# Performance work log

Hardware: AMD Instinct MI355X
Metric: run time of the kernel (lower is better)

The kernel has to match this reference:

```python
import jax, jax.numpy as jnp
import numpy as np
from jax import lax

SEQ_LEN = 1024
INPUT_DIM = 64
NUM_HIDDEN = 512
NUM_CLASSES = 10
BATCH = 256
SIGMA = 0.01


def setup_inputs() -> dict:
    key = jax.random.key(0)
    k_x, k_whx, k_whh, k_wph = jax.random.split(key, 4)
    x = jax.random.normal(k_x, (BATCH, SEQ_LEN, INPUT_DIM), dtype=jnp.float32)
    Whx = SIGMA * jax.random.normal(k_whx, (INPUT_DIM, NUM_HIDDEN), dtype=jnp.float32)
    Whh = SIGMA * jax.random.normal(k_whh, (NUM_HIDDEN, NUM_HIDDEN), dtype=jnp.float32)
    Wph = SIGMA * jax.random.normal(k_wph, (NUM_HIDDEN, NUM_CLASSES), dtype=jnp.float32)
    bh = jnp.zeros((NUM_HIDDEN, 1), dtype=jnp.float32)
    bp = jnp.zeros((NUM_CLASSES, 1), dtype=jnp.float32)
    return {"x": x, "Whx": Whx, "Whh": Whh, "Wph": Wph, "bh": bh, "bp": bp}


def reference(x, Whx, Whh, Wph, bh, bp):
    # x: [B, S, D]; h: [B, H]
    B = x.shape[0]
    H = Whh.shape[0]
    bh_row = bh[:, 0]  # per-hidden-unit bias (intended semantics of bh)
    bp_row = bp[:, 0]

    def step(h, xt):
        h_new = jnp.tanh(xt @ Whx + h @ Whh + bh_row)
        return h_new, None

    h0 = jnp.zeros((B, H), dtype=x.dtype)
    xs = jnp.swapaxes(x, 0, 1)  # [S, B, D] for scan over time
    h_final, _ = lax.scan(step, h0, xs)
    p = h_final @ Wph + bp_row  # [B, C]
    return p
```

## Files before the change

### kernel.cpp

```cpp
#include <hip/hip_runtime.h>
#include <hip/hip_bf16.h>
#include <hip/hip_fp8.h>
#include <cstdint>
#include <cstddef>


#define T_SEQ   1024
#define D_IN    64
#define H_DIM   512
#define NB      16
#define NBLK    16
#define NTW     4
#define KS_F16  10
#define KS_REG8 2
#define KS_LDS8 4
#define HSPLIT  320
#define APITCH  848
#define FP8OFF  640
#define ABUF_BYTES (2 * NB * APITCH)
#define WWAVE_BYTES (KS_LDS8 * 2 * 1024)
#define WLDS_BYTES (8 * WWAVE_BYTES)
#define SMEM_TOTAL (ABUF_BYTES + WLDS_BYTES)
#define WSCALE  256.0f
#define HSCALE  128.0f
#define UNSCALE (1.0f / 32768.0f)
#define U_BYTES ((size_t)T_SEQ * NBLK * 512 * 32)
#define TTP     64

typedef __attribute__((ext_vector_type(8))) short  short8;
typedef __attribute__((ext_vector_type(4))) short  short4v;
typedef __attribute__((ext_vector_type(4))) float  f32x4;
typedef __attribute__((ext_vector_type(4))) unsigned int uint4v;
typedef __attribute__((ext_vector_type(2))) unsigned int uint2v;

static __device__ __forceinline__ short f16b(float v) {
  return __builtin_bit_cast(short, (_Float16)v);
}
static __device__ __forceinline__ short bf16b(float v) {
  return __builtin_bit_cast(short, __float2bfloat16(v));
}
static __device__ __forceinline__ float f16f(unsigned short u) {
  return (float)__builtin_bit_cast(_Float16, (short)u);
}
static __device__ __forceinline__ unsigned int pk2h(float a, float b) {
#if defined(__has_builtin) && __has_builtin(__builtin_amdgcn_cvt_pkrtz)
  return __builtin_bit_cast(unsigned int, __builtin_amdgcn_cvt_pkrtz(a, b));
#else
  return (unsigned int)(unsigned short)f16b(a) |
         ((unsigned int)(unsigned short)f16b(b) << 16);
#endif
}
static __device__ __forceinline__ float fast_tanh(float x) {
  x = fminf(20.f, fmaxf(-20.f, x));
  const float t = __builtin_amdgcn_exp2f(x * 2.885390081777927f);
  return (t - 1.f) * __builtin_amdgcn_rcpf(t + 1.f);
}
static __device__ __forceinline__ unsigned char f32_to_fp8(float v) {
#if defined(__has_builtin) && __has_builtin(__builtin_amdgcn_cvt_pk_fp8_f32)
  const int r = __builtin_amdgcn_cvt_pk_fp8_f32(v, v, 0, false);
  return (unsigned char)(r & 0xff);
#else
  __hip_fp8_e4m3 f(v);
  return (unsigned char)f.__x;
#endif
}
static __device__ __forceinline__ unsigned int pk4fp8(float a, float b, float c, float d) {
#if defined(__has_builtin) && __has_builtin(__builtin_amdgcn_cvt_pk_fp8_f32)
  int r = __builtin_amdgcn_cvt_pk_fp8_f32(a, b, 0, false);
  r = __builtin_amdgcn_cvt_pk_fp8_f32(c, d, r, true);
  return (unsigned int)r;
#else
  return (unsigned int)f32_to_fp8(a) | ((unsigned int)f32_to_fp8(b) << 8) |
         ((unsigned int)f32_to_fp8(c) << 16) | ((unsigned int)f32_to_fp8(d) << 24);
#endif
}
static __device__ __forceinline__ float fp8_to_f32(unsigned char b) {
  __hip_fp8_e4m3 f;
  f.__x = (__hip_fp8_storage_t)b;
  return (float)f;
}

__global__ __launch_bounds__(512, 2)
void rnn_u_precompute(const float* __restrict__ x, const float* __restrict__ Whx,
                      const float* __restrict__ bh, char* __restrict__ U)
{
  const int tid  = threadIdx.x;
  const int lane = tid & 63;
  const int w    = tid >> 6;
  const int n16  = lane & 15;
  const int kq   = lane >> 4;
  const int wg   = blockIdx.x;
  const int cwave = w * 64;

  short8 wa[2][NTW];
  #pragma unroll
  for (int s = 0; s < 2; ++s) {
    #pragma unroll
    for (int nt = 0; nt < NTW; ++nt) {
      const int c = cwave + nt * 16 + n16;
      short8 f;
      #pragma unroll
      for (int j = 0; j < 8; ++j)
        f[j] = f16b(Whx[(size_t)(s * 32 + kq * 8 + j) * H_DIM + c]);
      wa[s][nt] = f;
    }
  }
  f32x4 bb[NTW];
  #pragma unroll
  for (int nt = 0; nt < NTW; ++nt) {
    #pragma unroll
    for (int i = 0; i < 4; ++i) bb[nt][i] = bh[cwave + nt * 16 + kq * 4 + i];
  }

  const int b = wg * NB + n16;
  const float* pxb = x + (size_t)b * T_SEQ * D_IN + kq * 8;
  const int t0 = blockIdx.y * TTP;

  f32x4 c0, c1, c2, c3;
  {
    const float* p = pxb + (size_t)t0 * D_IN;
    c0 = *(const f32x4*)p;        c1 = *(const f32x4*)(p + 4);
    c2 = *(const f32x4*)(p + 32); c3 = *(const f32x4*)(p + 36);
  }

  for (int tt = 0; tt < TTP; ++tt) {
    const int t = t0 + tt;
    f32x4 n0, n1, n2, n3;
    if (tt + 1 < TTP) {
      const float* p = pxb + (size_t)(t + 1) * D_IN;
      n0 = *(const f32x4*)p;        n1 = *(const f32x4*)(p + 4);
      n2 = *(const f32x4*)(p + 32); n3 = *(const f32x4*)(p + 36);
    }
    short8 xb0, xb1;
    xb0[0]=f16b(c0.x); xb0[1]=f16b(c0.y); xb0[2]=f16b(c0.z); xb0[3]=f16b(c0.w);
    xb0[4]=f16b(c1.x); xb0[5]=f16b(c1.y); xb0[6]=f16b(c1.z); xb0[7]=f16b(c1.w);
    xb1[0]=f16b(c2.x); xb1[1]=f16b(c2.y); xb1[2]=f16b(c2.z); xb1[3]=f16b(c2.w);
    xb1[4]=f16b(c3.x); xb1[5]=f16b(c3.y); xb1[6]=f16b(c3.z); xb1[7]=f16b(c3.w);

    f32x4 D[NTW];
    #pragma unroll
    for (int nt = 0; nt < NTW; ++nt) {
      D[nt] = bb[nt];
      D[nt] = __builtin_amdgcn_mfma_f32_16x16x32_f16(wa[0][nt], xb0, D[nt], 0, 0, 0);
      D[nt] = __builtin_amdgcn_mfma_f32_16x16x32_f16(wa[1][nt], xb1, D[nt], 0, 0, 0);
    }
    uint4v o0, o1;
    o0.x = pk2h(D[0][0], D[0][1]); o0.y = pk2h(D[0][2], D[0][3]);
    o0.z = pk2h(D[1][0], D[1][1]); o0.w = pk2h(D[1][2], D[1][3]);
    o1.x = pk2h(D[2][0], D[2][1]); o1.y = pk2h(D[2][2], D[2][3]);
    o1.z = pk2h(D[3][0], D[3][1]); o1.w = pk2h(D[3][2], D[3][3]);
    char* dst = U + (((size_t)t * NBLK + wg) * 512 + tid) * 32;
    *(uint4v*)dst = o0;
    *(uint4v*)(dst + 16) = o1;

    c0 = n0; c1 = n1; c2 = n2; c3 = n3;
  }
}

__global__ __launch_bounds__(512, 2)
void VanillaRNN_70025146794452_kernel(
    const float* __restrict__ Whh,
    const float* __restrict__ Wph,
    const float* __restrict__ bp,
    const char* __restrict__ U,
    float* __restrict__ out)
{
  const int tid  = threadIdx.x;
  const int lane = tid & 63;
  const int w    = tid >> 6;
  const int n16  = lane & 15;
  const int kq   = lane >> 4;
  const int rbase = blockIdx.x * NB;
  const int cwave = w * 64;

  extern __shared__ char smem[];
  char* Ab  = smem;
  char* Wlw = smem + ABUF_BYTES + w * WWAVE_BYTES;

  short8 wr[KS_F16][NTW];
  #pragma unroll
  for (int s = 0; s < KS_F16; ++s) {
    #pragma unroll
    for (int nt = 0; nt < NTW; ++nt) {
      const int c = cwave + nt * 16 + n16;
      short8 f;
      #pragma unroll
      for (int j = 0; j < 8; ++j)
        f[j] = f16b(Whh[(size_t)(s * 32 + kq * 8 + j) * H_DIM + c]);
      wr[s][nt] = f;
    }
  }
  long long wf8[KS_REG8][NTW];
  #pragma unroll
  for (int s = 0; s < KS_REG8; ++s) {
    #pragma unroll
    for (int nt = 0; nt < NTW; ++nt) {
      const int c  = cwave + nt * 16 + n16;
      const int k0 = (KS_F16 + s) * 32 + kq * 8;
      unsigned int lo = 0, hi = 0;
      #pragma unroll
      for (int bi = 0; bi < 4; ++bi) {
        lo |= ((unsigned int)f32_to_fp8(Whh[(size_t)(k0 + bi) * H_DIM + c] * WSCALE)) << (8 * bi);
        hi |= ((unsigned int)f32_to_fp8(Whh[(size_t)(k0 + 4 + bi) * H_DIM + c] * WSCALE)) << (8 * bi);
      }
      wf8[s][nt] = (long long)(((unsigned long long)hi << 32) | lo);
    }
  }
  for (int sl = 0; sl < KS_LDS8; ++sl) {
    for (int half = 0; half < 2; ++half) {
      const int k0 = (KS_F16 + KS_REG8 + sl) * 32 + kq * 8;
      unsigned int bqq[4];
      #pragma unroll
      for (int hh = 0; hh < 2; ++hh) {
        const int c = cwave + (2 * half + hh) * 16 + n16;
        #pragma unroll
        for (int u = 0; u < 2; ++u) {
          unsigned int acc = 0;
          #pragma unroll
          for (int bi = 0; bi < 4; ++bi)
            acc |= ((unsigned int)f32_to_fp8(Whh[(size_t)(k0 + u * 4 + bi) * H_DIM + c] * WSCALE)) << (8 * bi);
          bqq[hh * 2 + u] = acc;
        }
      }
      uint4v pk; pk.x = bqq[0]; pk.y = bqq[1]; pk.z = bqq[2]; pk.w = bqq[3];
      *(uint4v*)(Wlw + (size_t)(sl * 2 + half) * 1024 + lane * 16) = pk;
    }
  }

  for (int i = tid; i < ABUF_BYTES / 4; i += 512) ((int*)Ab)[i] = 0;
  uint4v Upf0, Upf1;
  {
    const char* up = U + (((size_t)0 * NBLK + blockIdx.x) * 512 + tid) * 32;
    Upf0 = *(const uint4v*)up;
    Upf1 = *(const uint4v*)(up + 16);
  }

  f32x4 C[NTW], C2[NTW];

  for (int t = 0; t < T_SEQ; ++t) {
    __syncthreads();
    char* Ac = Ab + (t & 1) * (NB * APITCH);
    char* An = Ab + ((t + 1) & 1) * (NB * APITCH);

    short8 hb = *(const short8*)(Ac + n16 * APITCH + 0 * 64 + kq * 16);

    C[0][0]=f16f(Upf0.x&0xffff); C[0][1]=f16f(Upf0.x>>16);
    C[0][2]=f16f(Upf0.y&0xffff); C[0][3]=f16f(Upf0.y>>16);
    C[1][0]=f16f(Upf0.z&0xffff); C[1][1]=f16f(Upf0.z>>16);
    C[1][2]=f16f(Upf0.w&0xffff); C[1][3]=f16f(Upf0.w>>16);
    C[2][0]=f16f(Upf1.x&0xffff); C[2][1]=f16f(Upf1.x>>16);
    C[2][2]=f16f(Upf1.y&0xffff); C[2][3]=f16f(Upf1.y>>16);
    C[3][0]=f16f(Upf1.z&0xffff); C[3][1]=f16f(Upf1.z>>16);
    C[3][2]=f16f(Upf1.w&0xffff); C[3][3]=f16f(Upf1.w>>16);
    #pragma unroll
    for (int nt = 0; nt < NTW; ++nt) C2[nt] = (f32x4){0.f, 0.f, 0.f, 0.f};

    {
      const int t1 = (t + 1 < T_SEQ) ? (t + 1) : (T_SEQ - 1);
      const char* up = U + (((size_t)t1 * NBLK + blockIdx.x) * 512 + tid) * 32;
      Upf0 = *(const uint4v*)up;
      Upf1 = *(const uint4v*)(up + 16);
    }

    #pragma unroll
    for (int s = 0; s < KS_F16; ++s) {
      const short8 a = hb;
      if (s + 1 < KS_F16)
        hb = *(const short8*)(Ac + n16 * APITCH + (s + 1) * 64 + kq * 16);
      #pragma unroll
      for (int nt = 0; nt < NTW; ++nt)
        C[nt] = __builtin_amdgcn_mfma_f32_16x16x32_f16(wr[s][nt], a, C[nt], 0, 0, 0);
    }
    #pragma unroll
    for (int s = 0; s < KS_REG8; ++s) {
      const long long h8 = *(const long long*)(Ac + n16 * APITCH + FP8OFF + s * 32 + kq * 8);
      #pragma unroll
      for (int nt = 0; nt < NTW; ++nt)
        C2[nt] = __builtin_amdgcn_mfma_f32_16x16x32_fp8_fp8(wf8[s][nt], h8, C2[nt], 0, 0, 0);
    }
    #pragma unroll
    for (int sl = 0; sl < KS_LDS8; ++sl) {
      const long long h8 = *(const long long*)(Ac + n16 * APITCH + FP8OFF + (KS_REG8 + sl) * 32 + kq * 8);
      const uint4v q0 = *(const uint4v*)(Wlw + (size_t)(sl * 2 + 0) * 1024 + lane * 16);
      const uint4v q1 = *(const uint4v*)(Wlw + (size_t)(sl * 2 + 1) * 1024 + lane * 16);
      const long long w0 = (long long)(((unsigned long long)q0.y << 32) | q0.x);
      const long long w1 = (long long)(((unsigned long long)q0.w << 32) | q0.z);
      const long long w2 = (long long)(((unsigned long long)q1.y << 32) | q1.x);
      const long long w3 = (long long)(((unsigned long long)q1.w << 32) | q1.z);
      C2[0] = __builtin_amdgcn_mfma_f32_16x16x32_fp8_fp8(w0, h8, C2[0], 0, 0, 0);
      C2[1] = __builtin_amdgcn_mfma_f32_16x16x32_fp8_fp8(w1, h8, C2[1], 0, 0, 0);
      C2[2] = __builtin_amdgcn_mfma_f32_16x16x32_fp8_fp8(w2, h8, C2[2], 0, 0, 0);
      C2[3] = __builtin_amdgcn_mfma_f32_16x16x32_fp8_fp8(w3, h8, C2[3], 0, 0, 0);
    }

    char* drow = An + n16 * APITCH;
    if (cwave < HSPLIT) {
      #pragma unroll
      for (int nt = 0; nt < NTW; ++nt) {
        const int c0 = cwave + nt * 16 + kq * 4;
        float v0 = fast_tanh(fmaf(C2[nt][0], UNSCALE, C[nt][0]));
        float v1 = fast_tanh(fmaf(C2[nt][1], UNSCALE, C[nt][1]));
        float v2 = fast_tanh(fmaf(C2[nt][2], UNSCALE, C[nt][2]));
        float v3 = fast_tanh(fmaf(C2[nt][3], UNSCALE, C[nt][3]));
        uint2v o; o.x = pk2h(v0, v1); o.y = pk2h(v2, v3);
        *(uint2v*)(drow + c0 * 2) = o;
      }
    } else {
      #pragma unroll
      for (int nt = 0; nt < NTW; ++nt) {
        const int c0 = cwave + nt * 16 + kq * 4;
        float v0 = fast_tanh(fmaf(C2[nt][0], UNSCALE, C[nt][0]));
        float v1 = fast_tanh(fmaf(C2[nt][1], UNSCALE, C[nt][1]));
        float v2 = fast_tanh(fmaf(C2[nt][2], UNSCALE, C[nt][2]));
        float v3 = fast_tanh(fmaf(C2[nt][3], UNSCALE, C[nt][3]));
        *(unsigned int*)(drow + FP8OFF + (c0 - HSPLIT)) =
            pk4fp8(v0 * HSCALE, v1 * HSCALE, v2 * HSCALE, v3 * HSCALE);
      }
    }
  }

  __syncthreads();
  if (tid < NB * 10) {
    const int r = tid / 10, c = tid % 10;
    const char* row = Ab + r * APITCH;
    float acc = bp[c];
    #pragma unroll 8
    for (int k = 0; k < HSPLIT; ++k)
      acc += f16f(*(const unsigned short*)(row + k * 2)) * Wph[k * 10 + c];
    #pragma unroll 8
    for (int k = HSPLIT; k < H_DIM; ++k)
      acc += fp8_to_f32((unsigned char)row[FP8OFF + (k - HSPLIT)]) * (1.f / HSCALE) * Wph[k * 10 + c];
    out[(size_t)(rbase + r) * 10 + c] = acc;
  }
}

#define FB_APITCH  1040
#define FB_FP8OFF  768
#define FB_ABUF    (2 * NB * FB_APITCH)
#define FB_WWAVE   (6 * 2 * 1024)
#define FB_SMEM    (FB_ABUF + 8 * FB_WWAVE)

__global__ __launch_bounds__(512, 2)
void rnn_fallback_kernel(
    const float* __restrict__ x, const float* __restrict__ Whx,
    const float* __restrict__ Whh, const float* __restrict__ Wph,
    const float* __restrict__ bh, const float* __restrict__ bp,
    float* __restrict__ out)
{
  const int tid = threadIdx.x, lane = tid & 63, w = tid >> 6;
  const int n16 = lane & 15, kq = lane >> 4;
  const int rbase = blockIdx.x * NB, cwave = w * 64;
  extern __shared__ char smem[];
  char* Ab  = smem;
  char* Wlw = smem + FB_ABUF + w * FB_WWAVE;

  short8 wr[12 * 4];
  #pragma unroll
  for (int s = 0; s < 12; ++s)
    #pragma unroll
    for (int nt = 0; nt < 4; ++nt) {
      const int c = cwave + nt * 16 + n16, k0 = s * 32 + kq * 8;
      short8 f;
      #pragma unroll
      for (int j = 0; j < 8; ++j) {
        const int k = k0 + j;
        const float* src = (k < D_IN) ? (Whx + (size_t)k * H_DIM + c)
                                      : (Whh + (size_t)(k - D_IN) * H_DIM + c);
        f[j] = bf16b(*src);
      }
      wr[s * 4 + nt] = f;
    }
  for (int s = 0; s < 6; ++s)
    for (int pp = 0; pp < 2; ++pp) {
      const int k0 = (12 + s) * 32 + kq * 8;
      unsigned int bq[4];
      #pragma unroll
      for (int half = 0; half < 2; ++half) {
        const int c = cwave + (2 * pp + half) * 16 + n16;
        #pragma unroll
        for (int u = 0; u < 2; ++u) {
          unsigned int acc = 0;
          #pragma unroll
          for (int bi = 0; bi < 4; ++bi)
            acc |= ((unsigned int)f32_to_fp8(Whh[(size_t)(k0 + u * 4 + bi - D_IN) * H_DIM + c] * WSCALE)) << (8 * bi);
          bq[half * 2 + u] = acc;
        }
      }
      uint4v pk; pk.x = bq[0]; pk.y = bq[1]; pk.z = bq[2]; pk.w = bq[3];
      *(uint4v*)(Wlw + (size_t)(s * 2 + pp) * 1024 + lane * 16) = pk;
    }
  float bhreg[4];
  #pragma unroll
  for (int nt = 0; nt < 4; ++nt) bhreg[nt] = bh[cwave + nt * 16 + n16];
  for (int i = tid; i < FB_ABUF / 4; i += 512) ((int*)Ab)[i] = 0;
  const int xr = (tid >> 4) & 15, xc4 = (tid & 15) * 4;
  if (tid < 256) {
    const f32x4 xv = *(const f32x4*)(x + ((size_t)(rbase + xr) * T_SEQ) * D_IN + xc4);
    short4v s4; s4[0]=bf16b(xv.x); s4[1]=bf16b(xv.y); s4[2]=bf16b(xv.z); s4[3]=bf16b(xv.w);
    *(short4v*)(Ab + xr * FB_APITCH + xc4 * 2) = s4;
  }
  f32x4 C[4], C2[4];
  for (int t = 0; t < T_SEQ; ++t) {
    __syncthreads();
    char* Ac = Ab + (t & 1) * (NB * FB_APITCH);
    char* An = Ab + ((t + 1) & 1) * (NB * FB_APITCH);
    const int t1 = (t + 1 < T_SEQ) ? (t + 1) : (T_SEQ - 1);
    f32x4 xv;
    if (tid < 256)
      xv = *(const f32x4*)(x + ((size_t)(rbase + xr) * T_SEQ + t1) * D_IN + xc4);
    #pragma unroll
    for (int nt = 0; nt < 4; ++nt) {
      C[nt] = (f32x4){0.f,0.f,0.f,0.f}; C2[nt] = (f32x4){0.f,0.f,0.f,0.f};
    }
    #pragma unroll
    for (int s = 0; s < 12; ++s) {
      const short8 a = *(const short8*)(Ac + n16 * FB_APITCH + s * 64 + kq * 16);
      #pragma unroll
      for (int nt = 0; nt < 4; ++nt)
        C[nt] = __builtin_amdgcn_mfma_f32_16x16x32_bf16(a, wr[s * 4 + nt], C[nt], 0, 0, 0);
    }
    #pragma unroll
    for (int s = 0; s < 6; ++s) {
      const long long a8 = *(const long long*)(Ac + n16 * FB_APITCH + FB_FP8OFF + s * 32 + kq * 8);
      #pragma unroll
      for (int pp = 0; pp < 2; ++pp) {
        const uint4v q = *(const uint4v*)(Wlw + (size_t)(s * 2 + pp) * 1024 + lane * 16);
        const long long b0 = (long long)(((unsigned long long)q.y << 32) | q.x);
        const long long b1 = (long long)(((unsigned long long)q.w << 32) | q.z);
        C2[2*pp]   = __builtin_amdgcn_mfma_f32_16x16x32_fp8_fp8(a8, b0, C2[2*pp],   0, 0, 0);
        C2[2*pp+1] = __builtin_amdgcn_mfma_f32_16x16x32_fp8_fp8(a8, b1, C2[2*pp+1], 0, 0, 0);
      }
    }
    if (tid < 256) {
      short4v s4; s4[0]=bf16b(xv.x); s4[1]=bf16b(xv.y); s4[2]=bf16b(xv.z); s4[3]=bf16b(xv.w);
      *(short4v*)(An + xr * FB_APITCH + xc4 * 2) = s4;
    }
    const int row0 = kq * 4;
    #pragma unroll
    for (int nt = 0; nt < 4; ++nt) {
      const int cbase = cwave + nt * 16;
      #pragma unroll
      for (int i = 0; i < 4; ++i) {
        const float v = fast_tanh(fmaf(C2[nt][i], UNSCALE, C[nt][i]) + bhreg[nt]);
        char* dst = An + (row0 + i) * FB_APITCH;
        if (cbase < 320) *(short*)(dst + 128 + (cbase + n16) * 2) = bf16b(v);
        else dst[FB_FP8OFF + (cbase + n16 - 320)] = f32_to_fp8(v * HSCALE);
      }
    }
  }
  __syncthreads();
  if (tid < NB * 10) {
    const int r = tid / 10, c = tid % 10;
    const char* row = Ab + r * FB_APITCH;
    float acc = bp[c];
    #pragma unroll 8
    for (int k = 0; k < 320; ++k) {
      const __hip_bfloat16 hb = __builtin_bit_cast(__hip_bfloat16, *(const short*)(row + 128 + k * 2));
      acc += __bfloat162float(hb) * Wph[k * 10 + c];
    }
    #pragma unroll 8
    for (int k = 320; k < H_DIM; ++k)
      acc += fp8_to_f32((unsigned char)row[FB_FP8OFF + (k - 320)]) * (1.f / HSCALE) * Wph[k * 10 + c];
    out[(size_t)(rbase + r) * 10 + c] = acc;
  }
}

extern "C" void kernel_launch(void* const* d_in, const int* in_sizes, int n_in,
                              void* d_out, int out_size, void* d_ws, size_t ws_size,
                              hipStream_t stream) {
  const float* x   = (const float*)d_in[0];
  const float* Whx = (const float*)d_in[1];
  const float* Whh = (const float*)d_in[2];
  const float* Wph = (const float*)d_in[3];
  const float* bh  = (const float*)d_in[4];
  const float* bp  = (const float*)d_in[5];
  float* out = (float*)d_out;

  if (ws_size >= U_BYTES) {
    char* U = (char*)d_ws;
    (void)hipFuncSetAttribute((const void*)VanillaRNN_70025146794452_kernel,
                              hipFuncAttributeMaxDynamicSharedMemorySize, SMEM_TOTAL);
    rnn_u_precompute<<<dim3(NBLK, T_SEQ / TTP), dim3(512), 0, stream>>>(x, Whx, bh, U);
    VanillaRNN_70025146794452_kernel<<<dim3(NBLK), dim3(512), SMEM_TOTAL, stream>>>(
        Whh, Wph, bp, U, out);
  } else {
    (void)hipFuncSetAttribute((const void*)rnn_fallback_kernel,
                              hipFuncAttributeMaxDynamicSharedMemorySize, FB_SMEM);
    rnn_fallback_kernel<<<dim3(NBLK), dim3(512), FB_SMEM, stream>>>(
        x, Whx, Whh, Wph, bh, bp, out);
  }
}
```

Before: 1.887 ms.

## Split each RNN batch group across two workgroups with global-memory flag exchange

Each 16-row batch group is now handled by a pair of workgroups, each computing half of the hidden columns, so 32 CUs run instead of 16. The partners swap their new hidden-state halves every timestep through a double-buffered global exchange buffer and spin on release/acquire flags. The U precompute layout changes to match the per-half column split. Each step now pays a cross-CU handoff through global memory. Spin loops have a bounded timeout that could silently produce wrong results if the partner workgroups are not co-resident.

After: 4.978 ms. +163.8%, slower.

```diff
diff --git a/kernel.cpp b/kernel.cpp
--- a/kernel.cpp
+++ b/kernel.cpp
@@ -18,20 +18,25 @@
 #define APITCH  848
 #define FP8OFF  640
 #define ABUF_BYTES (2 * NB * APITCH)
-#define WWAVE_BYTES (KS_LDS8 * 2 * 1024)
-#define WLDS_BYTES (8 * WWAVE_BYTES)
-#define SMEM_TOTAL (ABUF_BYTES + WLDS_BYTES)
+#define WWAVE2  (KS_LDS8 * 1024)
+#define WLDS2   (8 * WWAVE2)
+#define SMEM2   (ABUF_BYTES + WLDS2)
 #define WSCALE  256.0f
 #define HSCALE  128.0f
 #define UNSCALE (1.0f / 32768.0f)
-#define U_BYTES ((size_t)T_SEQ * NBLK * 512 * 32)
+#define U_BYTES ((size_t)T_SEQ * NBLK * 2 * 8192)
+#define USTEP   ((size_t)NBLK * 2 * 8192)
 #define TTP     64
+#define NPB     32
 
 typedef __attribute__((ext_vector_type(8))) short  short8;
 typedef __attribute__((ext_vector_type(4))) short  short4v;
 typedef __attribute__((ext_vector_type(4))) float  f32x4;
 typedef __attribute__((ext_vector_type(4))) unsigned int uint4v;
 typedef __attribute__((ext_vector_type(2))) unsigned int uint2v;
+
+__device__ int g_flags[NPB];
+__device__ __align__(16) char g_exch[NPB][2][8192];
 
 static __device__ __forceinline__ short f16b(float v) {
   return __builtin_bit_cast(short, (_Float16)v);
@@ -123,6 +128,9 @@
     c2 = *(const f32x4*)(p + 32); c3 = *(const f32x4*)(p + 36);
   }
 
+  char* dbase = U + ((size_t)(wg * 2 + (w >> 2))) * 8192 +
+                ((size_t)((w & 3) * 128 + lane)) * 16;
+
   for (int tt = 0; tt < TTP; ++tt) {
     const int t = t0 + tt;
     f32x4 n0, n1, n2, n3;
@@ -149,9 +157,9 @@
     o0.z = pk2h(D[1][0], D[1][1]); o0.w = pk2h(D[1][2], D[1][3]);
     o1.x = pk2h(D[2][0], D[2][1]); o1.y = pk2h(D[2][2], D[2][3]);
     o1.z = pk2h(D[3][0], D[3][1]); o1.w = pk2h(D[3][2], D[3][3]);
-    char* dst = U + (((size_t)t * NBLK + wg) * 512 + tid) * 32;
+    char* dst = dbase + (size_t)t * USTEP;
     *(uint4v*)dst = o0;
-    *(uint4v*)(dst + 16) = o1;
+    *(uint4v*)(dst + 1024) = o1;
 
     c0 = n0; c1 = n1; c2 = n2; c3 = n3;
   }
@@ -170,18 +178,22 @@
   const int w    = tid >> 6;
   const int n16  = lane & 15;
   const int kq   = lane >> 4;
-  const int rbase = blockIdx.x * NB;
-  const int cwave = w * 64;
+  const int bid  = blockIdx.x;
+  const int bg   = bid & 15;
+  const int hf   = bid >> 4;
+  const int pb   = bid ^ 16;
+  const int rbase = bg * NB;
+  const int cwave = hf * 256 + w * 32;
 
   extern __shared__ char smem[];
   char* Ab  = smem;
-  char* Wlw = smem + ABUF_BYTES + w * WWAVE_BYTES;
-
-  short8 wr[KS_F16][NTW];
+  char* Wlw = smem + ABUF_BYTES + w * WWAVE2;
+
+  short8 wr[KS_F16][2];
   #pragma unroll
   for (int s = 0; s < KS_F16; ++s) {
     #pragma unroll
-    for (int nt = 0; nt < NTW; ++nt) {
+    for (int nt = 0; nt < 2; ++nt) {
       const int c = cwave + nt * 16 + n16;
       short8 f;
       #pragma unroll
@@ -190,147 +202,203 @@
       wr[s][nt] = f;
     }
   }
-  long long wf8[KS_REG8][NTW];
+  long long wf8[KS_REG8][2];
   #pragma unroll
   for (int s = 0; s < KS_REG8; ++s) {
     #pragma unroll
-    for (int nt = 0; nt < NTW; ++nt) {
+    for (int nt = 0; nt < 2; ++nt) {
       const int c  = cwave + nt * 16 + n16;
       const int k0 = (KS_F16 + s) * 32 + kq * 8;
-      unsigned int lo = 0, hi = 0;
+      unsigned lo = 0, hi = 0;
       #pragma unroll
       for (int bi = 0; bi < 4; ++bi) {
-        lo |= ((unsigned int)f32_to_fp8(Whh[(size_t)(k0 + bi) * H_DIM + c] * WSCALE)) << (8 * bi);
-        hi |= ((unsigned int)f32_to_fp8(Whh[(size_t)(k0 + 4 + bi) * H_DIM + c] * WSCALE)) << (8 * bi);
+        lo |= ((unsigned)f32_to_fp8(Whh[(size_t)(k0 + bi) * H_DIM + c] * WSCALE)) << (8 * bi);
+        hi |= ((unsigned)f32_to_fp8(Whh[(size_t)(k0 + 4 + bi) * H_DIM + c] * WSCALE)) << (8 * bi);
       }
       wf8[s][nt] = (long long)(((unsigned long long)hi << 32) | lo);
     }
   }
   for (int sl = 0; sl < KS_LDS8; ++sl) {
-    for (int half = 0; half < 2; ++half) {
-      const int k0 = (KS_F16 + KS_REG8 + sl) * 32 + kq * 8;
-      unsigned int bqq[4];
-      #pragma unroll
-      for (int hh = 0; hh < 2; ++hh) {
-        const int c = cwave + (2 * half + hh) * 16 + n16;
+    const int k0 = (KS_F16 + KS_REG8 + sl) * 32 + kq * 8;
+    unsigned b4[4];
+    #pragma unroll
+    for (int nt = 0; nt < 2; ++nt) {
+      const int c = cwave + nt * 16 + n16;
+      #pragma unroll
+      for (int u = 0; u < 2; ++u) {
+        unsigned acc = 0;
         #pragma unroll
-        for (int u = 0; u < 2; ++u) {
-          unsigned int acc = 0;
-          #pragma unroll
-          for (int bi = 0; bi < 4; ++bi)
-            acc |= ((unsigned int)f32_to_fp8(Whh[(size_t)(k0 + u * 4 + bi) * H_DIM + c] * WSCALE)) << (8 * bi);
-          bqq[hh * 2 + u] = acc;
-        }
-      }
-      uint4v pk; pk.x = bqq[0]; pk.y = bqq[1]; pk.z = bqq[2]; pk.w = bqq[3];
-      *(uint4v*)(Wlw + (size_t)(sl * 2 + half) * 1024 + lane * 16) = pk;
-    }
-  }
+        for (int bi = 0; bi < 4; ++bi)
+          acc |= ((unsigned)f32_to_fp8(Whh[(size_t)(k0 + u * 4 + bi) * H_DIM + c] * WSCALE)) << (8 * bi);
+        b4[nt * 2 + u] = acc;
+      }
+    }
+    uint4v pk; pk.x = b4[0]; pk.y = b4[1]; pk.z = b4[2]; pk.w = b4[3];
+    *(uint4v*)(Wlw + (size_t)sl * 1024 + lane * 16) = pk;
+  }
+
+  int rrow, roff; bool ract;
+  if (hf == 0) {
+    ract = tid < 320; rrow = tid / 20; roff = 512 + (tid % 20) * 16;
+  } else {
+    ract = true;  rrow = tid >> 5;     roff = (tid & 31) * 16;
+  }
+
+  const char* Ubase   = U + ((size_t)(bg * 2 + hf)) * 8192 + (size_t)tid * 16;
+  char* exw_base      = &g_exch[bid][0][0];
+  const char* exr_base = &g_exch[pb][0][0];
 
   for (int i = tid; i < ABUF_BYTES / 4; i += 512) ((int*)Ab)[i] = 0;
-  uint4v Upf0, Upf1;
-  {
-    const char* up = U + (((size_t)0 * NBLK + blockIdx.x) * 512 + tid) * 32;
-    Upf0 = *(const uint4v*)up;
-    Upf1 = *(const uint4v*)(up + 16);
-  }
-
-  f32x4 C[NTW], C2[NTW];
+  uint4v Upf = *(const uint4v*)Ubase;
+  __syncthreads();
+
+  f32x4 C[2], C2[2];
 
   for (int t = 0; t < T_SEQ; ++t) {
-    __syncthreads();
     char* Ac = Ab + (t & 1) * (NB * APITCH);
     char* An = Ab + ((t + 1) & 1) * (NB * APITCH);
 
-    short8 hb = *(const short8*)(Ac + n16 * APITCH + 0 * 64 + kq * 16);
-
-    C[0][0]=f16f(Upf0.x&0xffff); C[0][1]=f16f(Upf0.x>>16);
-    C[0][2]=f16f(Upf0.y&0xffff); C[0][3]=f16f(Upf0.y>>16);
-    C[1][0]=f16f(Upf0.z&0xffff); C[1][1]=f16f(Upf0.z>>16);
-    C[1][2]=f16f(Upf0.w&0xffff); C[1][3]=f16f(Upf0.w>>16);
-    C[2][0]=f16f(Upf1.x&0xffff); C[2][1]=f16f(Upf1.x>>16);
-    C[2][2]=f16f(Upf1.y&0xffff); C[2][3]=f16f(Upf1.y>>16);
-    C[3][0]=f16f(Upf1.z&0xffff); C[3][1]=f16f(Upf1.z>>16);
-    C[3][2]=f16f(Upf1.w&0xffff); C[3][3]=f16f(Upf1.w>>16);
-    #pragma unroll
-    for (int nt = 0; nt < NTW; ++nt) C2[nt] = (f32x4){0.f, 0.f, 0.f, 0.f};
+    int fv = 0;
+    if (t > 0)
+      fv = __hip_atomic_load(&g_flags[pb], __ATOMIC_RELAXED, __HIP_MEMORY_SCOPE_AGENT);
+
+    C[0][0] = f16f(Upf.x & 0xffff); C[0][1] = f16f(Upf.x >> 16);
+    C[0][2] = f16f(Upf.y & 0xffff); C[0][3] = f16f(Upf.y >> 16);
+    C[1][0] = f16f(Upf.z & 0xffff); C[1][1] = f16f(Upf.z >> 16);
+    C[1][2] = f16f(Upf.w & 0xffff); C[1][3] = f16f(Upf.w >> 16);
+    C2[0] = (f32x4){0.f, 0.f, 0.f, 0.f};
+    C2[1] = (f32x4){0.f, 0.f, 0.f, 0.f};
 
     {
       const int t1 = (t + 1 < T_SEQ) ? (t + 1) : (T_SEQ - 1);
-      const char* up = U + (((size_t)t1 * NBLK + blockIdx.x) * 512 + tid) * 32;
-      Upf0 = *(const uint4v*)up;
-      Upf1 = *(const uint4v*)(up + 16);
-    }
-
-    #pragma unroll
-    for (int s = 0; s < KS_F16; ++s) {
-      const short8 a = hb;
-      if (s + 1 < KS_F16)
-        hb = *(const short8*)(Ac + n16 * APITCH + (s + 1) * 64 + kq * 16);
-      #pragma unroll
-      for (int nt = 0; nt < NTW; ++nt)
-        C[nt] = __builtin_amdgcn_mfma_f32_16x16x32_f16(wr[s][nt], a, C[nt], 0, 0, 0);
-    }
-    #pragma unroll
-    for (int s = 0; s < KS_REG8; ++s) {
-      const long long h8 = *(const long long*)(Ac + n16 * APITCH + FP8OFF + s * 32 + kq * 8);
-      #pragma unroll
-      for (int nt = 0; nt < NTW; ++nt)
-        C2[nt] = __builtin_amdgcn_mfma_f32_16x16x32_fp8_fp8(wf8[s][nt], h8, C2[nt], 0, 0, 0);
-    }
-    #pragma unroll
-    for (int sl = 0; sl < KS_LDS8; ++sl) {
-      const long long h8 = *(const long long*)(Ac + n16 * APITCH + FP8OFF + (KS_REG8 + sl) * 32 + kq * 8);
-      const uint4v q0 = *(const uint4v*)(Wlw + (size_t)(sl * 2 + 0) * 1024 + lane * 16);
-      const uint4v q1 = *(const uint4v*)(Wlw + (size_t)(sl * 2 + 1) * 1024 + lane * 16);
-      const long long w0 = (long long)(((unsigned long long)q0.y << 32) | q0.x);
-      const long long w1 = (long long)(((unsigned long long)q0.w << 32) | q0.z);
-      const long long w2 = (long long)(((unsigned long long)q1.y << 32) | q1.x);
-      const long long w3 = (long long)(((unsigned long long)q1.w << 32) | q1.z);
-      C2[0] = __builtin_amdgcn_mfma_f32_16x16x32_fp8_fp8(w0, h8, C2[0], 0, 0, 0);
-      C2[1] = __builtin_amdgcn_mfma_f32_16x16x32_fp8_fp8(w1, h8, C2[1], 0, 0, 0);
-      C2[2] = __builtin_amdgcn_mfma_f32_16x16x32_fp8_fp8(w2, h8, C2[2], 0, 0, 0);
-      C2[3] = __builtin_amdgcn_mfma_f32_16x16x32_fp8_fp8(w3, h8, C2[3], 0, 0, 0);
+      Upf = *(const uint4v*)(Ubase + (size_t)t1 * USTEP);
+    }
+
+    if (hf == 0) {
+      #pragma unroll
+      for (int s = 0; s < 8; ++s) {
+        const short8 a = *(const short8*)(Ac + n16 * APITCH + s * 64 + kq * 16);
+        C[0] = __builtin_amdgcn_mfma_f32_16x16x32_f16(wr[s][0], a, C[0], 0, 0, 0);
+        C[1] = __builtin_amdgcn_mfma_f32_16x16x32_f16(wr[s][1], a, C[1], 0, 0, 0);
+      }
+    } else {
+      #pragma unroll
+      for (int s = 8; s < KS_F16; ++s) {
+        const short8 a = *(const short8*)(Ac + n16 * APITCH + s * 64 + kq * 16);
+        C[0] = __builtin_amdgcn_mfma_f32_16x16x32_f16(wr[s][0], a, C[0], 0, 0, 0);
+        C[1] = __builtin_amdgcn_mfma_f32_16x16x32_f16(wr[s][1], a, C[1], 0, 0, 0);
+      }
+      #pragma unroll
+      for (int s = 0; s < KS_REG8; ++s) {
+        const long long h8 = *(const long long*)(Ac + n16 * APITCH + FP8OFF + s * 32 + kq * 8);
+        C2[0] = __builtin_amdgcn_mfma_f32_16x16x32_fp8_fp8(wf8[s][0], h8, C2[0], 0, 0, 0);
+        C2[1] = __builtin_amdgcn_mfma_f32_16x16x32_fp8_fp8(wf8[s][1], h8, C2[1], 0, 0, 0);
+      }
+      #pragma unroll
+      for (int sl = 0; sl < KS_LDS8; ++sl) {
+        const long long h8 = *(const long long*)(Ac + n16 * APITCH + FP8OFF + (KS_REG8 + sl) * 32 + kq * 8);
+        const uint4v q = *(const uint4v*)(Wlw + (size_t)sl * 1024 + lane * 16);
+        const long long w0 = (long long)(((unsigned long long)q.y << 32) | q.x);
+        const long long w1 = (long long)(((unsigned long long)q.w << 32) | q.z);
+        C2[0] = __builtin_amdgcn_mfma_f32_16x16x32_fp8_fp8(w0, h8, C2[0], 0, 0, 0);
+        C2[1] = __builtin_amdgcn_mfma_f32_16x16x32_fp8_fp8(w1, h8, C2[1], 0, 0, 0);
+      }
+    }
+
+    if (t > 0) {
+      unsigned spins = 0;
+      while (fv < t) {
+        fv = __hip_atomic_load(&g_flags[pb], __ATOMIC_RELAXED, __HIP_MEMORY_SCOPE_AGENT);
+        if (++spins > (1u << 20)) break;
+      }
+      __builtin_amdgcn_fence(__ATOMIC_ACQUIRE, "agent");
+      if (ract) {
+        const uint4v pay = *(const uint4v*)(exr_base + ((size_t)(t & 1) << 13) + (size_t)tid * 16);
+        *(uint4v*)(Ac + rrow * APITCH + roff) = pay;
+      }
+    }
+    __syncthreads();
+
+    if (hf == 0) {
+      #pragma unroll
+      for (int s = 8; s < KS_F16; ++s) {
+        const short8 a = *(const short8*)(Ac + n16 * APITCH + s * 64 + kq * 16);
+        C[0] = __builtin_amdgcn_mfma_f32_16x16x32_f16(wr[s][0], a, C[0], 0, 0, 0);
+        C[1] = __builtin_amdgcn_mfma_f32_16x16x32_f16(wr[s][1], a, C[1], 0, 0, 0);
+      }
+      #pragma unroll
+      for (int s = 0; s < KS_REG8; ++s) {
+        const long long h8 = *(const long long*)(Ac + n16 * APITCH + FP8OFF + s * 32 + kq * 8);
+        C2[0] = __builtin_amdgcn_mfma_f32_16x16x32_fp8_fp8(wf8[s][0], h8, C2[0], 0, 0, 0);
+        C2[1] = __builtin_amdgcn_mfma_f32_16x16x32_fp8_fp8(wf8[s][1], h8, C2[1], 0, 0, 0);
+      }
+      #pragma unroll
+      for (int sl = 0; sl < KS_LDS8; ++sl) {
+        const long long h8 = *(const long long*)(Ac + n16 * APITCH + FP8OFF + (KS_REG8 + sl) * 32 + kq * 8);
+        const uint4v q = *(const uint4v*)(Wlw + (size_t)sl * 1024 + lane * 16);
+        const long long w0 = (long long)(((unsigned long long)q.y << 32) | q.x);
+        const long long w1 = (long long)(((unsigned long long)q.w << 32) | q.z);
+        C2[0] = __builtin_amdgcn_mfma_f32_16x16x32_fp8_fp8(w0, h8, C2[0], 0, 0, 0);
+        C2[1] = __builtin_amdgcn_mfma_f32_16x16x32_fp8_fp8(w1, h8, C2[1], 0, 0, 0);
+      }
+    } else {
+      #pragma unroll
+      for (int s = 0; s < 8; ++s) {
+        const short8 a = *(const short8*)(Ac + n16 * APITCH + s * 64 + kq * 16);
+        C[0] = __builtin_amdgcn_mfma_f32_16x16x32_f16(wr[s][0], a, C[0], 0, 0, 0);
+        C[1] = __builtin_amdgcn_mfma_f32_16x16x32_f16(wr[s][1], a, C[1], 0, 0, 0);
+      }
     }
 
     char* drow = An + n16 * APITCH;
-    if (cwave < HSPLIT) {
-      #pragma unroll
-      for (int nt = 0; nt < NTW; ++nt) {
-        const int c0 = cwave + nt * 16 + kq * 4;
-        float v0 = fast_tanh(fmaf(C2[nt][0], UNSCALE, C[nt][0]));
-        float v1 = fast_tanh(fmaf(C2[nt][1], UNSCALE, C[nt][1]));
-        float v2 = fast_tanh(fmaf(C2[nt][2], UNSCALE, C[nt][2]));
-        float v3 = fast_tanh(fmaf(C2[nt][3], UNSCALE, C[nt][3]));
+    char* exw  = exw_base + ((size_t)((t + 1) & 1) << 13);
+    #pragma unroll
+    for (int nt = 0; nt < 2; ++nt) {
+      const int c0 = cwave + nt * 16 + kq * 4;
+      const float v0 = fast_tanh(fmaf(C2[nt][0], UNSCALE, C[nt][0]));
+      const float v1 = fast_tanh(fmaf(C2[nt][1], UNSCALE, C[nt][1]));
+      const float v2 = fast_tanh(fmaf(C2[nt][2], UNSCALE, C[nt][2]));
+      const float v3 = fast_tanh(fmaf(C2[nt][3], UNSCALE, C[nt][3]));
+      if (c0 < HSPLIT) {
         uint2v o; o.x = pk2h(v0, v1); o.y = pk2h(v2, v3);
         *(uint2v*)(drow + c0 * 2) = o;
-      }
-    } else {
-      #pragma unroll
-      for (int nt = 0; nt < NTW; ++nt) {
-        const int c0 = cwave + nt * 16 + kq * 4;
-        float v0 = fast_tanh(fmaf(C2[nt][0], UNSCALE, C[nt][0]));
-        float v1 = fast_tanh(fmaf(C2[nt][1], UNSCALE, C[nt][1]));
-        float v2 = fast_tanh(fmaf(C2[nt][2], UNSCALE, C[nt][2]));
-        float v3 = fast_tanh(fmaf(C2[nt][3], UNSCALE, C[nt][3]));
-        *(unsigned int*)(drow + FP8OFF + (c0 - HSPLIT)) =
-            pk4fp8(v0 * HSCALE, v1 * HSCALE, v2 * HSCALE, v3 * HSCALE);
-      }
-    }
-  }
-
-  __syncthreads();
-  if (tid < NB * 10) {
-    const int r = tid / 10, c = tid % 10;
-    const char* row = Ab + r * APITCH;
-    float acc = bp[c];
-    #pragma unroll 8
-    for (int k = 0; k < HSPLIT; ++k)
-      acc += f16f(*(const unsigned short*)(row + k * 2)) * Wph[k * 10 + c];
-    #pragma unroll 8
-    for (int k = HSPLIT; k < H_DIM; ++k)
-      acc += fp8_to_f32((unsigned char)row[FP8OFF + (k - HSPLIT)]) * (1.f / HSCALE) * Wph[k * 10 + c];
-    out[(size_t)(rbase + r) * 10 + c] = acc;
+        if (hf == 0) *(uint2v*)(exw + n16 * 512 + c0 * 2) = o;
+        else         *(uint2v*)(exw + n16 * 320 + (c0 - 256) * 2) = o;
+      } else {
+        const unsigned pj = pk4fp8(v0 * HSCALE, v1 * HSCALE, v2 * HSCALE, v3 * HSCALE);
+        *(unsigned*)(drow + FP8OFF + (c0 - HSPLIT)) = pj;
+        *(unsigned*)(exw + n16 * 320 + 128 + (c0 - HSPLIT)) = pj;
+      }
+    }
+
+    __syncthreads();
+    if (tid == 0)
+      __hip_atomic_store(&g_flags[bid], t + 1, __ATOMIC_RELEASE, __HIP_MEMORY_SCOPE_AGENT);
+  }
+
+  if (hf == 0) {
+    int fv; unsigned spins = 0;
+    do {
+      fv = __hip_atomic_load(&g_flags[pb], __ATOMIC_RELAXED, __HIP_MEMORY_SCOPE_AGENT);
+    } while (fv < T_SEQ && ++spins < (1u << 20));
+    __builtin_amdgcn_fence(__ATOMIC_ACQUIRE, "agent");
+    if (ract) {
+      const uint4v pay = *(const uint4v*)(exr_base + (size_t)tid * 16);
+      *(uint4v*)(Ab + rrow * APITCH + roff) = pay;
+    }
+    __syncthreads();
+    if (tid < NB * 10) {
+      const int r = tid / 10, c = tid % 10;
+      const char* row = Ab + r * APITCH;
+      float acc = bp[c];
+      #pragma unroll 8
+      for (int k = 0; k < HSPLIT; ++k)
+        acc += f16f(*(const unsigned short*)(row + k * 2)) * Wph[k * 10 + c];
+      #pragma unroll 8
+      for (int k = HSPLIT; k < H_DIM; ++k)
+        acc += fp8_to_f32((unsigned char)row[FP8OFF + (k - HSPLIT)]) * (1.f / HSCALE) * Wph[k * 10 + c];
+      out[(size_t)(rbase + r) * 10 + c] = acc;
+    }
   }
 }
 
@@ -477,16 +545,21 @@
   float* out = (float*)d_out;
 
   if (ws_size >= U_BYTES) {
-    char* U = (char*)d_ws;
-    (void)hipFuncSetAttribute((const void*)VanillaRNN_70025146794452_kernel,
-                              hipFuncAttributeMaxDynamicSharedMemorySize, SMEM_TOTAL);
-    rnn_u_precompute<<<dim3(NBLK, T_SEQ / TTP), dim3(512), 0, stream>>>(x, Whx, bh, U);
-    VanillaRNN_70025146794452_kernel<<<dim3(NBLK), dim3(512), SMEM_TOTAL, stream>>>(
-        Whh, Wph, bp, U, out);
-  } else {
-    (void)hipFuncSetAttribute((const void*)rnn_fallback_kernel,
-                              hipFuncAttributeMaxDynamicSharedMemorySize, FB_SMEM);
-    rnn_fallback_kernel<<<dim3(NBLK), dim3(512), FB_SMEM, stream>>>(
-        x, Whx, Whh, Wph, bh, bp, out);
-  }
-}
+    static void* flags_addr = nullptr;
+    if (!flags_addr) (void)hipGetSymbolAddress(&flags_addr, HIP_SYMBOL(g_flags));
+    if (flags_addr) {
+      char* Uws = (char*)d_ws;
+      (void)hipMemsetAsync(flags_addr, 0, sizeof(int) * NPB, stream);
+      (void)hipFuncSetAttribute((const void*)VanillaRNN_70025146794452_kernel,
+                                hipFuncAttributeMaxDynamicSharedMemorySize, SMEM2);
+      rnn_u_precompute<<<dim3(NBLK, T_SEQ / TTP), dim3(512), 0, stream>>>(x, Whx, bh, Uws);
+      VanillaRNN_70025146794452_kernel<<<dim3(NPB), dim3(512), SMEM2, stream>>>(
+          Whh, Wph, bp, Uws, out);
+      return;
+    }
+  }
+  (void)hipFuncSetAttribute((const void*)rnn_fallback_kernel,
+                            hipFuncAttributeMaxDynamicSharedMemorySize, FB_SMEM);
+  rnn_fallback_kernel<<<dim3(NBLK), dim3(512), FB_SMEM, stream>>>(
+      x, Whx, Whh, Wph, bh, bp, out);
+}
```

## Replace per-step block barrier with per-wave LDS flags and triple buffering

Applied to the files above, without the earlier changes.

Removes the __syncthreads at the top of every timestep. Each wave now publishes a release flag once it has written its slice of the new hidden state. Consumers do an acquire-spin on the producing wave's flag just before the MFMA region that reads that slice, and each wave starts with its own slice so its first region needs no wait. The hidden-state buffer goes from double to triple buffering so a wave that is one step ahead cannot overwrite data a slower wave is still reading. This lets waves overlap their work across steps, at the cost of spin-loop polling, a bounded spin timeout, s_setprio hints and a larger LDS footprint.

Result: slower. 2.176 ms (+15.3%).

```diff
diff --git a/kernel.cpp b/kernel.cpp
--- a/kernel.cpp
+++ b/kernel.cpp
@@ -17,10 +17,12 @@
 #define HSPLIT  320
 #define APITCH  848
 #define FP8OFF  640
-#define ABUF_BYTES (2 * NB * APITCH)
+#define ABUF3   (3 * NB * APITCH)
 #define WWAVE_BYTES (KS_LDS8 * 2 * 1024)
 #define WLDS_BYTES (8 * WWAVE_BYTES)
-#define SMEM_TOTAL (ABUF_BYTES + WLDS_BYTES)
+#define WLDS_OFF  ABUF3
+#define FLAGS_OFF (ABUF3 + WLDS_BYTES)
+#define SMEM_TOTAL (FLAGS_OFF + 64)
 #define WSCALE  256.0f
 #define HSCALE  128.0f
 #define UNSCALE (1.0f / 32768.0f)
@@ -156,6 +158,67 @@
     c0 = n0; c1 = n1; c2 = n2; c3 = n3;
   }
 }
+
+
+#define MF16(sA) do {                                                          \
+    const short8 a_ = *(const short8*)(Ac + n16 * APITCH + (sA) * 64 + kq * 16);\
+    C[0] = __builtin_amdgcn_mfma_f32_16x16x32_f16(wr[sA][0], a_, C[0], 0, 0, 0);\
+    C[1] = __builtin_amdgcn_mfma_f32_16x16x32_f16(wr[sA][1], a_, C[1], 0, 0, 0);\
+    C[2] = __builtin_amdgcn_mfma_f32_16x16x32_f16(wr[sA][2], a_, C[2], 0, 0, 0);\
+    C[3] = __builtin_amdgcn_mfma_f32_16x16x32_f16(wr[sA][3], a_, C[3], 0, 0, 0);\
+  } while (0)
+
+#define MR8(s8) do {                                                           \
+    const long long h8_ = *(const long long*)(Ac + n16 * APITCH + FP8OFF + (s8) * 32 + kq * 8); \
+    C2[0] = __builtin_amdgcn_mfma_f32_16x16x32_fp8_fp8(wf8[s8][0], h8_, C2[0], 0, 0, 0); \
+    C2[1] = __builtin_amdgcn_mfma_f32_16x16x32_fp8_fp8(wf8[s8][1], h8_, C2[1], 0, 0, 0); \
+    C2[2] = __builtin_amdgcn_mfma_f32_16x16x32_fp8_fp8(wf8[s8][2], h8_, C2[2], 0, 0, 0); \
+    C2[3] = __builtin_amdgcn_mfma_f32_16x16x32_fp8_fp8(wf8[s8][3], h8_, C2[3], 0, 0, 0); \
+  } while (0)
+
+#define ML8(sl) do {                                                           \
+    const long long h8_ = *(const long long*)(Ac + n16 * APITCH + FP8OFF + (KS_REG8 + (sl)) * 32 + kq * 8); \
+    const uint4v q0_ = *(const uint4v*)(Wlw + (size_t)((sl) * 2 + 0) * 1024 + lane * 16); \
+    const uint4v q1_ = *(const uint4v*)(Wlw + (size_t)((sl) * 2 + 1) * 1024 + lane * 16); \
+    const long long w0_ = (long long)(((unsigned long long)q0_.y << 32) | q0_.x); \
+    const long long w1_ = (long long)(((unsigned long long)q0_.w << 32) | q0_.z); \
+    const long long w2_ = (long long)(((unsigned long long)q1_.y << 32) | q1_.x); \
+    const long long w3_ = (long long)(((unsigned long long)q1_.w << 32) | q1_.z); \
+    C2[0] = __builtin_amdgcn_mfma_f32_16x16x32_fp8_fp8(w0_, h8_, C2[0], 0, 0, 0); \
+    C2[1] = __builtin_amdgcn_mfma_f32_16x16x32_fp8_fp8(w1_, h8_, C2[1], 0, 0, 0); \
+    C2[2] = __builtin_amdgcn_mfma_f32_16x16x32_fp8_fp8(w2_, h8_, C2[2], 0, 0, 0); \
+    C2[3] = __builtin_amdgcn_mfma_f32_16x16x32_fp8_fp8(w3_, h8_, C2[3], 0, 0, 0); \
+  } while (0)
+
+#define REGION_MFMA_0() do { MF16(0); MF16(1); } while (0)
+#define REGION_MFMA_1() do { MF16(2); MF16(3); } while (0)
+#define REGION_MFMA_2() do { MF16(4); MF16(5); } while (0)
+#define REGION_MFMA_3() do { MF16(6); MF16(7); } while (0)
+#define REGION_MFMA_4() do { MF16(8); MF16(9); } while (0)
+#define REGION_MFMA_5() do { MR8(0); MR8(1); } while (0)
+#define REGION_MFMA_6() do { ML8(0); ML8(1); } while (0)
+#define REGION_MFMA_7() do { ML8(2); ML8(3); } while (0)
+
+#define REGION(r, CHK) do {                                                    \
+    if (CHK) {                                                                 \
+      int fv_ = __hip_atomic_load(&flags[r], __ATOMIC_ACQUIRE,                 \
+                                  __HIP_MEMORY_SCOPE_WORKGROUP);               \
+      if (fv_ < t) {                                                           \
+        unsigned sp_ = 0;                                                      \
+        do {                                                                   \
+          fv_ = __hip_atomic_load(&flags[r], __ATOMIC_ACQUIRE,                 \
+                                  __HIP_MEMORY_SCOPE_WORKGROUP);               \
+        } while (fv_ < t && ++sp_ < (1u << 22));                               \
+        __builtin_amdgcn_sched_barrier(0);                                     \
+      }                                                                        \
+    }                                                                          \
+    REGION_MFMA_##r();                                                         \
+  } while (0)
+
+#define BODY(R0,R1,R2,R3,R4,R5,R6,R7) do {                                     \
+    REGION(R0, false); REGION(R1, true); REGION(R2, true); REGION(R3, true);   \
+    REGION(R4, true);  REGION(R5, true); REGION(R6, true); REGION(R7, true);   \
+  } while (0)
 
 __global__ __launch_bounds__(512, 2)
 void VanillaRNN_70025146794452_kernel(
@@ -175,7 +238,8 @@
 
   extern __shared__ char smem[];
   char* Ab  = smem;
-  char* Wlw = smem + ABUF_BYTES + w * WWAVE_BYTES;
+  char* Wlw = smem + WLDS_OFF + w * WWAVE_BYTES;
+  int*  flags = (int*)(smem + FLAGS_OFF);
 
   short8 wr[KS_F16][NTW];
   #pragma unroll
@@ -227,22 +291,21 @@
     }
   }
 
-  for (int i = tid; i < ABUF_BYTES / 4; i += 512) ((int*)Ab)[i] = 0;
+  for (int i = tid; i < ABUF3 / 4; i += 512) ((int*)Ab)[i] = 0;
+  if (tid < 8) flags[tid] = 0;
   uint4v Upf0, Upf1;
   {
     const char* up = U + (((size_t)0 * NBLK + blockIdx.x) * 512 + tid) * 32;
     Upf0 = *(const uint4v*)up;
     Upf1 = *(const uint4v*)(up + 16);
   }
+  __syncthreads();
 
   f32x4 C[NTW], C2[NTW];
 
   for (int t = 0; t < T_SEQ; ++t) {
-    __syncthreads();
-    char* Ac = Ab + (t & 1) * (NB * APITCH);
-    char* An = Ab + ((t + 1) & 1) * (NB * APITCH);
-
-    short8 hb = *(const short8*)(Ac + n16 * APITCH + 0 * 64 + kq * 16);
+    char* Ac = Ab + (t % 3) * (NB * APITCH);
+    char* An = Ab + ((t + 1) % 3) * (NB * APITCH);
 
     C[0][0]=f16f(Upf0.x&0xffff); C[0][1]=f16f(Upf0.x>>16);
     C[0][2]=f16f(Upf0.y&0xffff); C[0][3]=f16f(Upf0.y>>16);
@@ -262,36 +325,18 @@
       Upf1 = *(const uint4v*)(up + 16);
     }
 
-    #pragma unroll
-    for (int s = 0; s < KS_F16; ++s) {
-      const short8 a = hb;
-      if (s + 1 < KS_F16)
-        hb = *(const short8*)(Ac + n16 * APITCH + (s + 1) * 64 + kq * 16);
-      #pragma unroll
-      for (int nt = 0; nt < NTW; ++nt)
-        C[nt] = __builtin_amdgcn_mfma_f32_16x16x32_f16(wr[s][nt], a, C[nt], 0, 0, 0);
-    }
-    #pragma unroll
-    for (int s = 0; s < KS_REG8; ++s) {
-      const long long h8 = *(const long long*)(Ac + n16 * APITCH + FP8OFF + s * 32 + kq * 8);
-      #pragma unroll
-      for (int nt = 0; nt < NTW; ++nt)
-        C2[nt] = __builtin_amdgcn_mfma_f32_16x16x32_fp8_fp8(wf8[s][nt], h8, C2[nt], 0, 0, 0);
-    }
-    #pragma unroll
-    for (int sl = 0; sl < KS_LDS8; ++sl) {
-      const long long h8 = *(const long long*)(Ac + n16 * APITCH + FP8OFF + (KS_REG8 + sl) * 32 + kq * 8);
-      const uint4v q0 = *(const uint4v*)(Wlw + (size_t)(sl * 2 + 0) * 1024 + lane * 16);
-      const uint4v q1 = *(const uint4v*)(Wlw + (size_t)(sl * 2 + 1) * 1024 + lane * 16);
-      const long long w0 = (long long)(((unsigned long long)q0.y << 32) | q0.x);
-      const long long w1 = (long long)(((unsigned long long)q0.w << 32) | q0.z);
-      const long long w2 = (long long)(((unsigned long long)q1.y << 32) | q1.x);
-      const long long w3 = (long long)(((unsigned long long)q1.w << 32) | q1.z);
-      C2[0] = __builtin_amdgcn_mfma_f32_16x16x32_fp8_fp8(w0, h8, C2[0], 0, 0, 0);
-      C2[1] = __builtin_amdgcn_mfma_f32_16x16x32_fp8_fp8(w1, h8, C2[1], 0, 0, 0);
-      C2[2] = __builtin_amdgcn_mfma_f32_16x16x32_fp8_fp8(w2, h8, C2[2], 0, 0, 0);
-      C2[3] = __builtin_amdgcn_mfma_f32_16x16x32_fp8_fp8(w3, h8, C2[3], 0, 0, 0);
-    }
+    __builtin_amdgcn_s_setprio(1);
+    switch (w) {
+      case 0: BODY(0,1,2,3,4,5,6,7); break;
+      case 1: BODY(1,2,3,4,5,6,7,0); break;
+      case 2: BODY(2,3,4,5,6,7,0,1); break;
+      case 3: BODY(3,4,5,6,7,0,1,2); break;
+      case 4: BODY(4,5,6,7,0,1,2,3); break;
+      case 5: BODY(5,6,7,0,1,2,3,4); break;
+      case 6: BODY(6,7,0,1,2,3,4,5); break;
+      default: BODY(7,0,1,2,3,4,5,6); break;
+    }
+    __builtin_amdgcn_s_setprio(0);
 
     char* drow = An + n16 * APITCH;
     if (cwave < HSPLIT) {
@@ -317,12 +362,16 @@
             pk4fp8(v0 * HSCALE, v1 * HSCALE, v2 * HSCALE, v3 * HSCALE);
       }
     }
+
+    if (lane == 0)
+      __hip_atomic_store(&flags[w], t + 1, __ATOMIC_RELEASE,
+                         __HIP_MEMORY_SCOPE_WORKGROUP);
   }
 
   __syncthreads();
   if (tid < NB * 10) {
     const int r = tid / 10, c = tid % 10;
-    const char* row = Ab + r * APITCH;
+    const char* row = Ab + (T_SEQ % 3) * (NB * APITCH) + r * APITCH;
     float acc = bp[c];
     #pragma unroll 8
     for (int k = 0; k < HSPLIT; ++k)
```
